# Optimization experiments

Measured on AMD Instinct MI355X. Metric: run time of the kernel, lower is better.

## Reference

```python
import jax, jax.numpy as jnp
import numpy as np

D_MODEL = 1024
NHEAD = 16
HEAD_DIM = D_MODEL // NHEAD
D_FF = 4096
LN_EPS = 1e-5


def _layernorm(x, gamma, beta):
    mu = jnp.mean(x, axis=-1, keepdims=True)
    var = jnp.mean(jnp.square(x - mu), axis=-1, keepdims=True)
    return (x - mu) * jax.lax.rsqrt(var + LN_EPS) * gamma + beta


def setup_inputs() -> dict:
    key = jax.random.key(0)
    ks = jax.random.split(key, 16)
    s = 1.0 / np.sqrt(D_MODEL)
    sf = 1.0 / np.sqrt(D_FF)
    inp = {
        "src": jax.random.normal(ks[0], (2, 2048, D_MODEL), dtype=jnp.float32),
        # projection weights stored [in, out]
        "Wq": jax.random.uniform(ks[1], (D_MODEL, D_MODEL), minval=-s, maxval=s),
        "bq": jax.random.uniform(ks[2], (D_MODEL,), minval=-s, maxval=s),
        "Wk": jax.random.uniform(ks[3], (D_MODEL, D_MODEL), minval=-s, maxval=s),
        "bk": jax.random.uniform(ks[4], (D_MODEL,), minval=-s, maxval=s),
        "Wv": jax.random.uniform(ks[5], (D_MODEL, D_MODEL), minval=-s, maxval=s),
        "bv": jax.random.uniform(ks[6], (D_MODEL,), minval=-s, maxval=s),
        "Wo": jax.random.uniform(ks[7], (D_MODEL, D_MODEL), minval=-s, maxval=s),
        "bo": jax.random.uniform(ks[8], (D_MODEL,), minval=-s, maxval=s),
        "W1": jax.random.uniform(ks[9], (D_MODEL, D_FF), minval=-s, maxval=s),
        "b1": jax.random.uniform(ks[10], (D_FF,), minval=-s, maxval=s),
        "W2": jax.random.uniform(ks[11], (D_FF, D_MODEL), minval=-sf, maxval=sf),
        "b2": jax.random.uniform(ks[12], (D_MODEL,), minval=-sf, maxval=sf),
        "gamma1": jnp.ones((D_MODEL,), jnp.float32),
        "beta1": jnp.zeros((D_MODEL,), jnp.float32),
        "gamma2": jnp.ones((D_MODEL,), jnp.float32),
        "beta2": jnp.zeros((D_MODEL,), jnp.float32),
    }
    return inp


def reference(src, Wq, bq, Wk, bk, Wv, bv, Wo, bo, W1, b1, W2, b2,
              gamma1, beta1, gamma2, beta2):
    B, L, D = src.shape
    H, Hd = NHEAD, HEAD_DIM
    # QKV projections -> [B, H, L, Hd]
    def split_heads(x):
        return x.reshape(B, L, H, Hd).transpose(0, 2, 1, 3)
    Q = split_heads(src @ Wq + bq)
    K = split_heads(src @ Wk + bk)
    V = split_heads(src @ Wv + bv)
    # attention (dropout is eval-mode identity)
    scores = jnp.einsum("bhqd,bhkd->bhqk", Q, K) / np.sqrt(Hd)
    probs = jax.nn.softmax(scores, axis=-1)
    attn = jnp.einsum("bhqk,bhkd->bhqd", probs, V)
    attn = attn.transpose(0, 2, 1, 3).reshape(B, L, D)
    attn = attn @ Wo + bo
    x = _layernorm(src + attn, gamma1, beta1)
    ff = jax.nn.gelu(x @ W1 + b1, approximate=False) @ W2 + b2
    return _layernorm(x + ff, gamma2, beta2)
```

## Files before the change

kernel.cpp:

```cpp
#include <hip/hip_runtime.h>
#include <cstdint>
#include <cstddef>

using short8 = short __attribute__((ext_vector_type(8)));
using f32x4  = float __attribute__((ext_vector_type(4)));

__device__ __forceinline__ unsigned short f2bf(float f) {
  unsigned int u = __float_as_uint(f);
  u += 0x7fffu + ((u >> 16) & 1u);
  return (unsigned short)(u >> 16);
}
__device__ __forceinline__ float bf2f(unsigned short s) {
  return __uint_as_float(((unsigned int)s) << 16);
}
__device__ __forceinline__ unsigned int pack_bf16_rhu(float lo, float hi) {
  unsigned int a = __float_as_uint(lo) + 0x8000u;
  unsigned int b = __float_as_uint(hi) + 0x8000u;
  return __builtin_amdgcn_perm(b, a, 0x07060302u);
}
__device__ __forceinline__ void async16(const void* g, void* l) {
  __builtin_amdgcn_global_load_lds(
      (const __attribute__((address_space(1))) unsigned int*)g,
      (__attribute__((address_space(3))) unsigned int*)l, 16, 0, 0);
}

#define D_MODEL 1024
#define NHEAD   16
#define HEADD   64
#define SEQL    2048
#define NTOK    4096
#define QSCALE  0.18033688011112042f

__global__ __launch_bounds__(256) void cvt_f32_bf16(const float* __restrict__ in,
                                                    unsigned short* __restrict__ out,
                                                    int n4) {
  int i = blockIdx.x * 256 + threadIdx.x;
  if (i >= n4) return;
  float4 v = ((const float4*)in)[i];
  union { unsigned long long u; unsigned int ui[2]; } pk;
  pk.ui[0] = pack_bf16_rhu(v.x, v.y);
  pk.ui[1] = pack_bf16_rhu(v.z, v.w);
  ((unsigned long long*)out)[i] = pk.u;
}

struct TransTab {
  const float* src[6];
  unsigned short* dst[6];
  int R[6], C[6], start[6], shift[6];
};

__global__ __launch_bounds__(256) void transpose_all(TransTab tt) {
  int id = blockIdx.x, m = 0;
#pragma unroll
  for (int i = 1; i < 6; ++i) if (id >= tt.start[i]) m = i;
  const int local = id - tt.start[m];
  const int R = tt.R[m], C = tt.C[m];
  const int bc = (local & ((1 << tt.shift[m]) - 1)) * 32;
  const int br = (local >> tt.shift[m]) * 32;
  const float* in = tt.src[m];
  unsigned short* out = tt.dst[m];
  __shared__ float tile[32][33];
  const int tx = threadIdx.x & 31, ty = threadIdx.x >> 5;
#pragma unroll
  for (int i = 0; i < 32; i += 8)
    tile[ty + i][tx] = in[(size_t)(br + ty + i) * C + bc + tx];
  __syncthreads();
#pragma unroll
  for (int i = 0; i < 32; i += 8)
    out[(size_t)(bc + ty + i) * R + br + tx] = f2bf(tile[tx][ty + i]);
}

template <int MODE>
__global__ __launch_bounds__(256, 4)
void gemm_bt(const unsigned short* __restrict__ A, const unsigned short* __restrict__ B,
             int M, int N, int K, int Kstride,
             const float* __restrict__ bias0, const float* __restrict__ bias1,
             const float* __restrict__ bias2,
             float* __restrict__ outF, unsigned short* __restrict__ outB,
             unsigned short* __restrict__ outQ, unsigned short* __restrict__ outK,
             unsigned short* __restrict__ outVT) {
  __shared__ __align__(16) short sA[128 * 64];
  __shared__ __align__(16) short sB[128 * 64];
  const int tid = threadIdx.x, wave = tid >> 6, lane = tid & 63;
  const int quad = lane >> 4, l16 = lane & 15;
  const int bm = blockIdx.y * 128, bn = blockIdx.x * 128;
  const int koff = blockIdx.z * K;
  const int wr = (wave >> 1) * 64, wc = (wave & 1) * 64;
  const f32x4 zero4 = {0.f, 0.f, 0.f, 0.f};
  f32x4 acc[4][4];
#pragma unroll
  for (int i = 0; i < 4; ++i)
#pragma unroll
    for (int j = 0; j < 4; ++j) acc[i][j] = zero4;

  for (int kt = 0; kt < K; kt += 64) {
    __syncthreads();
#pragma unroll
    for (int j = 0; j < 4; ++j) {
      int c = (wave * 4 + j) * 64 + lane;
      int row = c >> 3, cp = c & 7;
      int gk = koff + kt + ((cp ^ (row & 7)) * 8);
      async16(A + (size_t)(bm + row) * Kstride + gk, &sA[(wave * 4 + j) * 512]);
      async16(B + (size_t)(bn + row) * Kstride + gk, &sB[(wave * 4 + j) * 512]);
    }
    __syncthreads();
#pragma unroll
    for (int kk = 0; kk < 2; ++kk) {
      short8 af[4], bfr[4];
#pragma unroll
      for (int i = 0; i < 4; ++i) {
        int ra = wr + i * 16 + l16;
        af[i] = *(const short8*)&sA[ra * 64 + (((kk * 4 + quad) ^ (ra & 7)) * 8)];
        int rb = wc + i * 16 + l16;
        bfr[i] = *(const short8*)&sB[rb * 64 + (((kk * 4 + quad) ^ (rb & 7)) * 8)];
      }
#pragma unroll
      for (int mi = 0; mi < 4; ++mi)
#pragma unroll
        for (int ni = 0; ni < 4; ++ni)
          acc[mi][ni] = __builtin_amdgcn_mfma_f32_16x16x32_bf16(af[mi], bfr[ni], acc[mi][ni], 0, 0, 0);
    }
  }

#pragma unroll
  for (int mi = 0; mi < 4; ++mi)
#pragma unroll
    for (int ni = 0; ni < 4; ++ni) {
      const int col = bn + wc + ni * 16 + l16;
      const int row0 = bm + wr + mi * 16 + quad * 4;
      if constexpr (MODE == 0) {
        const int b_ = row0 >> 11, l_ = row0 & 2047;
        if (col < 1024) {
          const int hh = col >> 6, dd = col & 63;
          const size_t o = (((size_t)(b_ * NHEAD + hh)) * SEQL + l_) * HEADD + dd;
#pragma unroll
          for (int r = 0; r < 4; ++r)
            outQ[o + (size_t)r * HEADD] = f2bf((acc[mi][ni][r] + bias0[col]) * QSCALE);
        } else if (col < 2048) {
          const int n2 = col - 1024, hh = n2 >> 6, dd = n2 & 63;
          const size_t o = (((size_t)(b_ * NHEAD + hh)) * SEQL + l_) * HEADD + dd;
#pragma unroll
          for (int r = 0; r < 4; ++r)
            outK[o + (size_t)r * HEADD] = f2bf(acc[mi][ni][r] + bias1[n2]);
        } else {
          const int n2 = col - 2048, hh = n2 >> 6, dd = n2 & 63;
          union { unsigned long long u; unsigned short us[4]; } pk;
#pragma unroll
          for (int r = 0; r < 4; ++r) pk.us[r] = f2bf(acc[mi][ni][r] + bias2[n2]);
          *(unsigned long long*)&outVT[(((size_t)(b_ * NHEAD + hh)) * HEADD + dd) * SEQL + l_] = pk.u;
        }
      } else if constexpr (MODE == 1) {
        float* o = outF + (size_t)blockIdx.z * M * N + (size_t)row0 * N + col;
#pragma unroll
        for (int r = 0; r < 4; ++r) o[(size_t)r * N] = acc[mi][ni][r];
      } else {
#pragma unroll
        for (int r = 0; r < 4; ++r) {
          float x = acc[mi][ni][r] + bias0[col];
          float x2 = x * x;
          float z = x * fmaf(0.102944f, x2, 2.302208f);
          float t = __builtin_amdgcn_exp2f(z);
          float gl = x - x * __builtin_amdgcn_rcpf(t + 1.0f);
          outB[(size_t)(row0 + r) * N + col] = f2bf(gl);
        }
      }
    }
}

__global__ __launch_bounds__(256)
void flash_attn(const unsigned short* __restrict__ Qb, const unsigned short* __restrict__ Kb,
                const unsigned short* __restrict__ VTb, unsigned short* __restrict__ attnA) {
  __shared__ __align__(16) short sV[64 * 128];
  __shared__ __align__(16) short sP[128 * 72];
  const int tid = threadIdx.x, wave = tid >> 6, lane = tid & 63;
  const int quad = lane >> 4, l16 = lane & 15;
  const int bh = blockIdx.y;
  const int q0 = blockIdx.x * 128;
  const size_t baseQK = (size_t)bh * SEQL * HEADD;
  const size_t baseV  = (size_t)bh * HEADD * SEQL;

  short8 qf[2][2];
#pragma unroll
  for (int mi = 0; mi < 2; ++mi)
#pragma unroll
    for (int kk = 0; kk < 2; ++kk) {
      int q = q0 + wave * 32 + mi * 16 + l16;
      qf[mi][kk] = *(const short8*)(Qb + baseQK + (size_t)q * HEADD + kk * 32 + quad * 8);
    }

  const f32x4 zero4 = {0.f, 0.f, 0.f, 0.f};
  f32x4 o_acc[2][4];
  float lsum[2] = {0.f, 0.f};
#pragma unroll
  for (int mi = 0; mi < 2; ++mi)
#pragma unroll
    for (int ni = 0; ni < 4; ++ni) o_acc[mi][ni] = zero4;

  for (int t0 = 0; t0 < SEQL; t0 += 128) {
    __syncthreads();
#pragma unroll
    for (int j = 0; j < 4; ++j) {
      int c = (wave * 4 + j) * 64 + lane;
      int d = c >> 4, cp = c & 15;
      int gl = (cp ^ (d & 15)) * 8;
      async16(VTb + baseV + (size_t)d * SEQL + t0 + gl, &sV[(wave * 4 + j) * 512]);
    }
    __syncthreads();

#pragma unroll
    for (int h = 0; h < 2; ++h) {
      f32x4 st[4][2];
#pragma unroll
      for (int kt = 0; kt < 4; ++kt)
#pragma unroll
        for (int mi = 0; mi < 2; ++mi) st[kt][mi] = zero4;
#pragma unroll
      for (int kt = 0; kt < 4; ++kt) {
        const unsigned short* kp =
            Kb + baseQK + (size_t)(t0 + h * 64 + kt * 16 + l16) * HEADD + quad * 8;
        short8 a0 = *(const short8*)(kp);
        short8 a1 = *(const short8*)(kp + 32);
#pragma unroll
        for (int mi = 0; mi < 2; ++mi) {
          st[kt][mi] = __builtin_amdgcn_mfma_f32_16x16x32_bf16(a0, qf[mi][0], st[kt][mi], 0, 0, 0);
          st[kt][mi] = __builtin_amdgcn_mfma_f32_16x16x32_bf16(a1, qf[mi][1], st[kt][mi], 0, 0, 0);
        }
      }
#pragma unroll
      for (int kt = 0; kt < 4; ++kt)
#pragma unroll
        for (int mi = 0; mi < 2; ++mi) {
          float e0 = __builtin_amdgcn_exp2f(st[kt][mi][0]);
          float e1 = __builtin_amdgcn_exp2f(st[kt][mi][1]);
          float e2 = __builtin_amdgcn_exp2f(st[kt][mi][2]);
          float e3 = __builtin_amdgcn_exp2f(st[kt][mi][3]);
          lsum[mi] += (e0 + e1) + (e2 + e3);
          int q = wave * 32 + mi * 16 + l16;
          union { unsigned long long u; unsigned int ui[2]; } pk;
          pk.ui[0] = pack_bf16_rhu(e0, e1);
          pk.ui[1] = pack_bf16_rhu(e2, e3);
          *(unsigned long long*)&sP[q * 72 + kt * 16 + quad * 4] = pk.u;
        }
#pragma unroll
      for (int c = 0; c < 2; ++c) {
        short8 pf[2];
#pragma unroll
        for (int mi = 0; mi < 2; ++mi) {
          int q = wave * 32 + mi * 16 + l16;
          pf[mi] = *(const short8*)&sP[q * 72 + c * 32 + quad * 8];
        }
#pragma unroll
        for (int ni = 0; ni < 4; ++ni) {
          int vrow = ni * 16 + l16;
          short8 vf = *(const short8*)&sV[vrow * 128 + (((h * 8 + c * 4 + quad) ^ (vrow & 15)) * 8)];
#pragma unroll
          for (int mi = 0; mi < 2; ++mi)
            o_acc[mi][ni] = __builtin_amdgcn_mfma_f32_16x16x32_bf16(pf[mi], vf, o_acc[mi][ni], 0, 0, 0);
        }
      }
    }
  }

#pragma unroll
  for (int mi = 0; mi < 2; ++mi) {
    lsum[mi] += __shfl_xor(lsum[mi], 16, 64);
    lsum[mi] += __shfl_xor(lsum[mi], 32, 64);
  }
  const int b_ = bh >> 4, hh = bh & 15;
#pragma unroll
  for (int mi = 0; mi < 2; ++mi)
#pragma unroll
    for (int r = 0; r < 4; ++r) {
      float inv = 1.0f / __shfl(lsum[mi], quad * 4 + r, 64);
      int qrow = q0 + wave * 32 + mi * 16 + quad * 4 + r;
      size_t orow = ((size_t)(b_ * SEQL + qrow)) * D_MODEL + hh * HEADD;
#pragma unroll
      for (int ni = 0; ni < 4; ++ni)
        attnA[orow + ni * 16 + l16] = f2bf(o_acc[mi][ni][r] * inv);
    }
}

__device__ __forceinline__ void ln_core(float x0, float x1, float x2, float x3,
                                        const float* gamma, const float* beta,
                                        int tid, float& y0, float& y1, float& y2, float& y3) {
  float s = x0 + x1 + x2 + x3;
  float q = x0 * x0 + x1 * x1 + x2 * x2 + x3 * x3;
#pragma unroll
  for (int m = 1; m < 64; m <<= 1) {
    s += __shfl_xor(s, m, 64);
    q += __shfl_xor(q, m, 64);
  }
  __shared__ float red[8];
  const int wv = tid >> 6, ln = tid & 63;
  if (ln == 0) { red[wv] = s; red[4 + wv] = q; }
  __syncthreads();
  float S = red[0] + red[1] + red[2] + red[3];
  float Q2 = red[4] + red[5] + red[6] + red[7];
  float mu = S * (1.0f / 1024.0f);
  float var = Q2 * (1.0f / 1024.0f) - mu * mu;
  float rstd = rsqrtf(var + 1e-5f);
  float4 g = ((const float4*)gamma)[tid];
  float4 b = ((const float4*)beta)[tid];
  y0 = (x0 - mu) * rstd * g.x + b.x;
  y1 = (x1 - mu) * rstd * g.y + b.y;
  y2 = (x2 - mu) * rstd * g.z + b.z;
  y3 = (x3 - mu) * rstd * g.w + b.w;
}

__global__ __launch_bounds__(256)
void ln_combine1(const float* __restrict__ p, int nsplit, const float* __restrict__ src,
                 const float* __restrict__ bias, const float* __restrict__ gamma,
                 const float* __restrict__ beta, unsigned short* __restrict__ outB) {
  const int t = blockIdx.x, tid = threadIdx.x;
  const size_t MN = (size_t)NTOK * 1024, base = (size_t)t * 1024;
  float4 a = ((const float4*)(p + base))[tid];
  for (int s = 1; s < nsplit; ++s) {
    float4 b4 = ((const float4*)(p + s * MN + base))[tid];
    a.x += b4.x; a.y += b4.y; a.z += b4.z; a.w += b4.w;
  }
  float4 s4 = ((const float4*)(src + base))[tid];
  float4 bi = ((const float4*)bias)[tid];
  float y0, y1, y2, y3;
  ln_core(a.x + s4.x + bi.x, a.y + s4.y + bi.y,
          a.z + s4.z + bi.z, a.w + s4.w + bi.w,
          gamma, beta, tid, y0, y1, y2, y3);
  union { unsigned long long u; unsigned int ui[2]; } pk;
  pk.ui[0] = (unsigned)f2bf(y0) | ((unsigned)f2bf(y1) << 16);
  pk.ui[1] = (unsigned)f2bf(y2) | ((unsigned)f2bf(y3) << 16);
  ((unsigned long long*)(outB + base))[tid] = pk.u;
}

__global__ __launch_bounds__(256)
void ln_combine2(const float* __restrict__ p, int nsplit, const unsigned short* __restrict__ resB,
                 const float* __restrict__ bias, const float* __restrict__ gamma,
                 const float* __restrict__ beta, float* __restrict__ outF) {
  const int t = blockIdx.x, tid = threadIdx.x;
  const size_t MN = (size_t)NTOK * 1024, base = (size_t)t * 1024;
  float4 a = ((const float4*)(p + base))[tid];
  for (int s = 1; s < nsplit; ++s) {
    float4 b4 = ((const float4*)(p + s * MN + base))[tid];
    a.x += b4.x; a.y += b4.y; a.z += b4.z; a.w += b4.w;
  }
  union { unsigned long long u; unsigned short us[4]; } r;
  r.u = ((const unsigned long long*)(resB + base))[tid];
  float4 bi = ((const float4*)bias)[tid];
  float y0, y1, y2, y3;
  ln_core(a.x + bf2f(r.us[0]) + bi.x, a.y + bf2f(r.us[1]) + bi.y,
          a.z + bf2f(r.us[2]) + bi.z, a.w + bf2f(r.us[3]) + bi.w,
          gamma, beta, tid, y0, y1, y2, y3);
  float4 o = {y0, y1, y2, y3};
  ((float4*)(outF + base))[tid] = o;
}

extern "C" void kernel_launch(void* const* d_in, const int* in_sizes, int n_in,
                              void* d_out, int out_size, void* d_ws, size_t ws_size,
                              hipStream_t stream) {
  const float* src    = (const float*)d_in[0];
  const float* Wq     = (const float*)d_in[1];
  const float* bq     = (const float*)d_in[2];
  const float* Wk     = (const float*)d_in[3];
  const float* bk     = (const float*)d_in[4];
  const float* Wv     = (const float*)d_in[5];
  const float* bv     = (const float*)d_in[6];
  const float* Wo     = (const float*)d_in[7];
  const float* bo     = (const float*)d_in[8];
  const float* W1     = (const float*)d_in[9];
  const float* b1     = (const float*)d_in[10];
  const float* W2     = (const float*)d_in[11];
  const float* b2     = (const float*)d_in[12];
  const float* gamma1 = (const float*)d_in[13];
  const float* beta1  = (const float*)d_in[14];
  const float* gamma2 = (const float*)d_in[15];
  const float* beta2  = (const float*)d_in[16];
  float* out = (float*)d_out;
  (void)in_sizes; (void)n_in; (void)out_size;

  char* p = (char*)d_ws;
  size_t used = 0;
  auto carve = [&](size_t n) {
    char* r = p; size_t a = (n + 255) & ~(size_t)255; p += a; used += a; return r;
  };
  unsigned short* srcB  = (unsigned short*)carve((size_t)NTOK * 1024 * 2);
  unsigned short* WqkvT = (unsigned short*)carve((size_t)3072 * 1024 * 2);
  unsigned short* WoT   = (unsigned short*)carve((size_t)1024 * 1024 * 2);
  unsigned short* W1T   = (unsigned short*)carve((size_t)4096 * 1024 * 2);
  unsigned short* W2T   = (unsigned short*)carve((size_t)1024 * 4096 * 2);
  unsigned short* Qb    = (unsigned short*)carve((size_t)NTOK * 1024 * 2);
  unsigned short* Kb    = (unsigned short*)carve((size_t)NTOK * 1024 * 2);
  unsigned short* VTb   = (unsigned short*)carve((size_t)NTOK * 1024 * 2);
  carve((size_t)NTOK * 1024 * 2);
  unsigned short* xln   = (unsigned short*)carve((size_t)NTOK * 1024 * 2);
  unsigned short* hmid  = (unsigned short*)carve((size_t)NTOK * 4096 * 2);
  unsigned short* attnA = srcB;
  float* partial2 = (float*)Qb;
  const size_t need4 = (size_t)NTOK * 1024 * 4 * 4;
  float* partial4 = (ws_size >= used + need4) ? (float*)carve(need4) : nullptr;
  const int nsplit = partial4 ? 4 : 2;
  float* partial = partial4 ? partial4 : partial2;

  cvt_f32_bf16<<<4096, 256, 0, stream>>>(src, srcB, NTOK * 1024 / 4);
  TransTab tt;
  tt.src[0] = Wq; tt.src[1] = Wk; tt.src[2] = Wv; tt.src[3] = Wo; tt.src[4] = W1; tt.src[5] = W2;
  tt.dst[0] = WqkvT; tt.dst[1] = WqkvT + 1024 * 1024; tt.dst[2] = WqkvT + 2 * 1024 * 1024;
  tt.dst[3] = WoT; tt.dst[4] = W1T; tt.dst[5] = W2T;
  for (int i = 0; i < 4; ++i) { tt.R[i] = 1024; tt.C[i] = 1024; tt.shift[i] = 5; }
  tt.R[4] = 1024; tt.C[4] = 4096; tt.shift[4] = 7;
  tt.R[5] = 4096; tt.C[5] = 1024; tt.shift[5] = 5;
  tt.start[0] = 0; tt.start[1] = 1024; tt.start[2] = 2048; tt.start[3] = 3072;
  tt.start[4] = 4096; tt.start[5] = 8192;
  transpose_all<<<12288, 256, 0, stream>>>(tt);

  gemm_bt<0><<<dim3(24, 32, 1), 256, 0, stream>>>(srcB, WqkvT, NTOK, 3072, 1024, 1024,
                                                  bq, bk, bv, nullptr, nullptr, Qb, Kb, VTb);
  flash_attn<<<dim3(16, 32), 256, 0, stream>>>(Qb, Kb, VTb, attnA);
  gemm_bt<1><<<dim3(8, 32, nsplit), 256, 0, stream>>>(attnA, WoT, NTOK, 1024, 1024 / nsplit, 1024,
                                                      nullptr, nullptr, nullptr, partial,
                                                      nullptr, nullptr, nullptr, nullptr);
  ln_combine1<<<NTOK, 256, 0, stream>>>(partial, nsplit, src, bo, gamma1, beta1, xln);
  gemm_bt<2><<<dim3(32, 32, 1), 256, 0, stream>>>(xln, W1T, NTOK, 4096, 1024, 1024,
                                                  b1, nullptr, nullptr, nullptr, hmid,
                                                  nullptr, nullptr, nullptr);
  gemm_bt<1><<<dim3(8, 32, nsplit), 256, 0, stream>>>(hmid, W2T, NTOK, 1024, 4096 / nsplit, 4096,
                                                      nullptr, nullptr, nullptr, partial,
                                                      nullptr, nullptr, nullptr, nullptr);
  ln_combine2<<<NTOK, 256, 0, stream>>>(partial, nsplit, xln, b2, gamma2, beta2, out);
}
```

Measured before the change: 391.9 us.

## Split attention keys across wave pairs, stage K/Q in LDS, fuse prep kernels

Flash attention now runs 512-thread blocks where pairs of waves split each 128-key tile and combine partial outputs and row sums through LDS at the end. Q and K tiles are loaded asynchronously into swizzled LDS instead of read per-wave from global memory. The bf16 conversion of src is merged into the weight transpose kernel to drop a launch, and the output-projection/FFN2 split-K is fixed at 2, removing the optional 4-way partial buffer. The key split adds a final reduction and more LDS use per block.

Result: faster. 338.1 us (-13.7%).

```diff
diff --git a/kernel.cpp b/kernel.cpp
--- a/kernel.cpp
+++ b/kernel.cpp
@@ -31,26 +31,28 @@
 #define NTOK    4096
 #define QSCALE  0.18033688011112042f
 
-__global__ __launch_bounds__(256) void cvt_f32_bf16(const float* __restrict__ in,
-                                                    unsigned short* __restrict__ out,
-                                                    int n4) {
-  int i = blockIdx.x * 256 + threadIdx.x;
-  if (i >= n4) return;
-  float4 v = ((const float4*)in)[i];
-  union { unsigned long long u; unsigned int ui[2]; } pk;
-  pk.ui[0] = pack_bf16_rhu(v.x, v.y);
-  pk.ui[1] = pack_bf16_rhu(v.z, v.w);
-  ((unsigned long long*)out)[i] = pk.u;
-}
-
 struct TransTab {
   const float* src[6];
   unsigned short* dst[6];
   int R[6], C[6], start[6], shift[6];
+  const float* cvt_in;
+  unsigned short* cvt_out;
 };
 
-__global__ __launch_bounds__(256) void transpose_all(TransTab tt) {
-  int id = blockIdx.x, m = 0;
+__global__ __launch_bounds__(256) void prep_all(TransTab tt) {
+  __shared__ float tile[32][33];
+  int id = blockIdx.x;
+  if (id < 4096) {
+    int i = id * 256 + threadIdx.x;
+    float4 v = ((const float4*)tt.cvt_in)[i];
+    union { unsigned long long u; unsigned int ui[2]; } pk;
+    pk.ui[0] = pack_bf16_rhu(v.x, v.y);
+    pk.ui[1] = pack_bf16_rhu(v.z, v.w);
+    ((unsigned long long*)tt.cvt_out)[i] = pk.u;
+    return;
+  }
+  id -= 4096;
+  int m = 0;
 #pragma unroll
   for (int i = 1; i < 6; ++i) if (id >= tt.start[i]) m = i;
   const int local = id - tt.start[m];
@@ -59,7 +61,6 @@
   const int br = (local >> tt.shift[m]) * 32;
   const float* in = tt.src[m];
   unsigned short* out = tt.dst[m];
-  __shared__ float tile[32][33];
   const int tx = threadIdx.x & 31, ty = threadIdx.x >> 5;
 #pragma unroll
   for (int i = 0; i < 32; i += 8)
@@ -167,25 +168,38 @@
     }
 }
 
-__global__ __launch_bounds__(256)
+__global__ __launch_bounds__(512, 4)
 void flash_attn(const unsigned short* __restrict__ Qb, const unsigned short* __restrict__ Kb,
                 const unsigned short* __restrict__ VTb, unsigned short* __restrict__ attnA) {
+  __shared__ __align__(16) short sK[128 * 64];
   __shared__ __align__(16) short sV[64 * 128];
-  __shared__ __align__(16) short sP[128 * 72];
+  __shared__ __align__(16) short sP[8 * 32 * 72];
+  __shared__ float lred[4][32];
   const int tid = threadIdx.x, wave = tid >> 6, lane = tid & 63;
   const int quad = lane >> 4, l16 = lane & 15;
+  const int wq = wave >> 1;
+  const int wk = wave & 1;
   const int bh = blockIdx.y;
   const int q0 = blockIdx.x * 128;
   const size_t baseQK = (size_t)bh * SEQL * HEADD;
   const size_t baseV  = (size_t)bh * HEADD * SEQL;
-
+  const int pbase = wave * (32 * 72);
+
+#pragma unroll
+  for (int j = 0; j < 2; ++j) {
+    int c = (wave * 2 + j) * 64 + lane;
+    int row = c >> 3, cp = c & 7;
+    int gk = (cp ^ (row & 7)) * 8;
+    async16(Qb + baseQK + (size_t)(q0 + row) * HEADD + gk, &sK[(wave * 2 + j) * 512]);
+  }
+  __syncthreads();
   short8 qf[2][2];
 #pragma unroll
   for (int mi = 0; mi < 2; ++mi)
 #pragma unroll
     for (int kk = 0; kk < 2; ++kk) {
-      int q = q0 + wave * 32 + mi * 16 + l16;
-      qf[mi][kk] = *(const short8*)(Qb + baseQK + (size_t)q * HEADD + kk * 32 + quad * 8);
+      int m = wq * 32 + mi * 16 + l16;
+      qf[mi][kk] = *(const short8*)&sK[m * 64 + (((kk * 4 + quad) ^ (m & 7)) * 8)];
     }
 
   const f32x4 zero4 = {0.f, 0.f, 0.f, 0.f};
@@ -199,64 +213,61 @@
   for (int t0 = 0; t0 < SEQL; t0 += 128) {
     __syncthreads();
 #pragma unroll
-    for (int j = 0; j < 4; ++j) {
-      int c = (wave * 4 + j) * 64 + lane;
-      int d = c >> 4, cp = c & 15;
-      int gl = (cp ^ (d & 15)) * 8;
-      async16(VTb + baseV + (size_t)d * SEQL + t0 + gl, &sV[(wave * 4 + j) * 512]);
+    for (int j = 0; j < 2; ++j) {
+      int c = (wave * 2 + j) * 64 + lane;
+      { int row = c >> 3, cp = c & 7;
+        int gk = (cp ^ (row & 7)) * 8;
+        async16(Kb + baseQK + (size_t)(t0 + row) * HEADD + gk, &sK[(wave * 2 + j) * 512]); }
+      { int d = c >> 4, cp = c & 15;
+        int gl = (cp ^ (d & 15)) * 8;
+        async16(VTb + baseV + (size_t)d * SEQL + t0 + gl, &sV[(wave * 2 + j) * 512]); }
     }
     __syncthreads();
 
-#pragma unroll
-    for (int h = 0; h < 2; ++h) {
-      f32x4 st[4][2];
-#pragma unroll
-      for (int kt = 0; kt < 4; ++kt)
-#pragma unroll
-        for (int mi = 0; mi < 2; ++mi) st[kt][mi] = zero4;
-#pragma unroll
-      for (int kt = 0; kt < 4; ++kt) {
-        const unsigned short* kp =
-            Kb + baseQK + (size_t)(t0 + h * 64 + kt * 16 + l16) * HEADD + quad * 8;
-        short8 a0 = *(const short8*)(kp);
-        short8 a1 = *(const short8*)(kp + 32);
-#pragma unroll
-        for (int mi = 0; mi < 2; ++mi) {
-          st[kt][mi] = __builtin_amdgcn_mfma_f32_16x16x32_bf16(a0, qf[mi][0], st[kt][mi], 0, 0, 0);
-          st[kt][mi] = __builtin_amdgcn_mfma_f32_16x16x32_bf16(a1, qf[mi][1], st[kt][mi], 0, 0, 0);
-        }
-      }
-#pragma unroll
-      for (int kt = 0; kt < 4; ++kt)
-#pragma unroll
-        for (int mi = 0; mi < 2; ++mi) {
-          float e0 = __builtin_amdgcn_exp2f(st[kt][mi][0]);
-          float e1 = __builtin_amdgcn_exp2f(st[kt][mi][1]);
-          float e2 = __builtin_amdgcn_exp2f(st[kt][mi][2]);
-          float e3 = __builtin_amdgcn_exp2f(st[kt][mi][3]);
-          lsum[mi] += (e0 + e1) + (e2 + e3);
-          int q = wave * 32 + mi * 16 + l16;
-          union { unsigned long long u; unsigned int ui[2]; } pk;
-          pk.ui[0] = pack_bf16_rhu(e0, e1);
-          pk.ui[1] = pack_bf16_rhu(e2, e3);
-          *(unsigned long long*)&sP[q * 72 + kt * 16 + quad * 4] = pk.u;
-        }
-#pragma unroll
-      for (int c = 0; c < 2; ++c) {
-        short8 pf[2];
-#pragma unroll
-        for (int mi = 0; mi < 2; ++mi) {
-          int q = wave * 32 + mi * 16 + l16;
-          pf[mi] = *(const short8*)&sP[q * 72 + c * 32 + quad * 8];
-        }
-#pragma unroll
-        for (int ni = 0; ni < 4; ++ni) {
-          int vrow = ni * 16 + l16;
-          short8 vf = *(const short8*)&sV[vrow * 128 + (((h * 8 + c * 4 + quad) ^ (vrow & 15)) * 8)];
-#pragma unroll
-          for (int mi = 0; mi < 2; ++mi)
-            o_acc[mi][ni] = __builtin_amdgcn_mfma_f32_16x16x32_bf16(pf[mi], vf, o_acc[mi][ni], 0, 0, 0);
-        }
+    f32x4 st[4][2];
+#pragma unroll
+    for (int kt = 0; kt < 4; ++kt)
+#pragma unroll
+      for (int mi = 0; mi < 2; ++mi) st[kt][mi] = zero4;
+#pragma unroll
+    for (int kt = 0; kt < 4; ++kt) {
+      int krow = wk * 64 + kt * 16 + l16;
+      short8 a0 = *(const short8*)&sK[krow * 64 + ((quad ^ (krow & 7)) * 8)];
+      short8 a1 = *(const short8*)&sK[krow * 64 + (((4 + quad) ^ (krow & 7)) * 8)];
+#pragma unroll
+      for (int mi = 0; mi < 2; ++mi) {
+        st[kt][mi] = __builtin_amdgcn_mfma_f32_16x16x32_bf16(a0, qf[mi][0], st[kt][mi], 0, 0, 0);
+        st[kt][mi] = __builtin_amdgcn_mfma_f32_16x16x32_bf16(a1, qf[mi][1], st[kt][mi], 0, 0, 0);
+      }
+    }
+#pragma unroll
+    for (int kt = 0; kt < 4; ++kt)
+#pragma unroll
+      for (int mi = 0; mi < 2; ++mi) {
+        float e0 = __builtin_amdgcn_exp2f(st[kt][mi][0]);
+        float e1 = __builtin_amdgcn_exp2f(st[kt][mi][1]);
+        float e2 = __builtin_amdgcn_exp2f(st[kt][mi][2]);
+        float e3 = __builtin_amdgcn_exp2f(st[kt][mi][3]);
+        lsum[mi] += (e0 + e1) + (e2 + e3);
+        union { unsigned long long u; unsigned int ui[2]; } pk;
+        pk.ui[0] = pack_bf16_rhu(e0, e1);
+        pk.ui[1] = pack_bf16_rhu(e2, e3);
+        *(unsigned long long*)&sP[pbase + (mi * 16 + l16) * 72 + kt * 16 + quad * 4] = pk.u;
+      }
+#pragma unroll
+    for (int c = 0; c < 2; ++c) {
+      short8 vf[4];
+#pragma unroll
+      for (int ni = 0; ni < 4; ++ni) {
+        int vrow = ni * 16 + l16;
+        vf[ni] = *(const short8*)&sV[vrow * 128 + (((wk * 8 + c * 4 + quad) ^ (vrow & 15)) * 8)];
+      }
+#pragma unroll
+      for (int mi = 0; mi < 2; ++mi) {
+        short8 pf = *(const short8*)&sP[pbase + (mi * 16 + l16) * 72 + c * 32 + quad * 8];
+#pragma unroll
+        for (int ni = 0; ni < 4; ++ni)
+          o_acc[mi][ni] = __builtin_amdgcn_mfma_f32_16x16x32_bf16(pf, vf[ni], o_acc[mi][ni], 0, 0, 0);
       }
     }
   }
@@ -266,18 +277,43 @@
     lsum[mi] += __shfl_xor(lsum[mi], 16, 64);
     lsum[mi] += __shfl_xor(lsum[mi], 32, 64);
   }
-  const int b_ = bh >> 4, hh = bh & 15;
-#pragma unroll
-  for (int mi = 0; mi < 2; ++mi)
-#pragma unroll
-    for (int r = 0; r < 4; ++r) {
-      float inv = 1.0f / __shfl(lsum[mi], quad * 4 + r, 64);
-      int qrow = q0 + wave * 32 + mi * 16 + quad * 4 + r;
-      size_t orow = ((size_t)(b_ * SEQL + qrow)) * D_MODEL + hh * HEADD;
+  __syncthreads();
+  float* op = (float*)sP;
+  if (wk == 1) {
+    float* dst = op + wq * (64 * 36);
+#pragma unroll
+    for (int mi = 0; mi < 2; ++mi)
 #pragma unroll
       for (int ni = 0; ni < 4; ++ni)
-        attnA[orow + ni * 16 + l16] = f2bf(o_acc[mi][ni][r] * inv);
-    }
+        *(f32x4*)&dst[(ni * 16 + l16) * 36 + mi * 16 + quad * 4] = o_acc[mi][ni];
+    if (quad == 0) {
+      lred[wq][l16] = lsum[0];
+      lred[wq][16 + l16] = lsum[1];
+    }
+  }
+  __syncthreads();
+  if (wk == 0) {
+    const float* srcp = op + wq * (64 * 36);
+    const int b_ = bh >> 4, hh = bh & 15;
+#pragma unroll
+    for (int mi = 0; mi < 2; ++mi) {
+      float ltot = lsum[mi] + lred[wq][mi * 16 + l16];
+#pragma unroll
+      for (int ni = 0; ni < 4; ++ni) {
+        f32x4 other = *(const f32x4*)&srcp[(ni * 16 + l16) * 36 + mi * 16 + quad * 4];
+        o_acc[mi][ni] += other;
+      }
+#pragma unroll
+      for (int r = 0; r < 4; ++r) {
+        float inv = 1.0f / __shfl(ltot, quad * 4 + r, 64);
+        int qrow = q0 + wq * 32 + mi * 16 + quad * 4 + r;
+        size_t orow = ((size_t)(b_ * SEQL + qrow)) * D_MODEL + hh * HEADD;
+#pragma unroll
+        for (int ni = 0; ni < 4; ++ni)
+          attnA[orow + ni * 16 + l16] = f2bf(o_acc[mi][ni][r] * inv);
+      }
+    }
+  }
 }
 
 __device__ __forceinline__ void ln_core(float x0, float x1, float x2, float x3,
@@ -308,16 +344,14 @@
 }
 
 __global__ __launch_bounds__(256)
-void ln_combine1(const float* __restrict__ p, int nsplit, const float* __restrict__ src,
+void ln_combine1(const float* __restrict__ p, const float* __restrict__ src,
                  const float* __restrict__ bias, const float* __restrict__ gamma,
                  const float* __restrict__ beta, unsigned short* __restrict__ outB) {
   const int t = blockIdx.x, tid = threadIdx.x;
   const size_t MN = (size_t)NTOK * 1024, base = (size_t)t * 1024;
   float4 a = ((const float4*)(p + base))[tid];
-  for (int s = 1; s < nsplit; ++s) {
-    float4 b4 = ((const float4*)(p + s * MN + base))[tid];
-    a.x += b4.x; a.y += b4.y; a.z += b4.z; a.w += b4.w;
-  }
+  float4 b4 = ((const float4*)(p + MN + base))[tid];
+  a.x += b4.x; a.y += b4.y; a.z += b4.z; a.w += b4.w;
   float4 s4 = ((const float4*)(src + base))[tid];
   float4 bi = ((const float4*)bias)[tid];
   float y0, y1, y2, y3;
@@ -331,16 +365,14 @@
 }
 
 __global__ __launch_bounds__(256)
-void ln_combine2(const float* __restrict__ p, int nsplit, const unsigned short* __restrict__ resB,
+void ln_combine2(const float* __restrict__ p, const unsigned short* __restrict__ resB,
                  const float* __restrict__ bias, const float* __restrict__ gamma,
                  const float* __restrict__ beta, float* __restrict__ outF) {
   const int t = blockIdx.x, tid = threadIdx.x;
   const size_t MN = (size_t)NTOK * 1024, base = (size_t)t * 1024;
   float4 a = ((const float4*)(p + base))[tid];
-  for (int s = 1; s < nsplit; ++s) {
-    float4 b4 = ((const float4*)(p + s * MN + base))[tid];
-    a.x += b4.x; a.y += b4.y; a.z += b4.z; a.w += b4.w;
-  }
+  float4 b4 = ((const float4*)(p + MN + base))[tid];
+  a.x += b4.x; a.y += b4.y; a.z += b4.z; a.w += b4.w;
   union { unsigned long long u; unsigned short us[4]; } r;
   r.u = ((const unsigned long long*)(resB + base))[tid];
   float4 bi = ((const float4*)bias)[tid];
@@ -373,13 +405,10 @@
   const float* gamma2 = (const float*)d_in[15];
   const float* beta2  = (const float*)d_in[16];
   float* out = (float*)d_out;
-  (void)in_sizes; (void)n_in; (void)out_size;
+  (void)in_sizes; (void)n_in; (void)out_size; (void)ws_size;
 
   char* p = (char*)d_ws;
-  size_t used = 0;
-  auto carve = [&](size_t n) {
-    char* r = p; size_t a = (n + 255) & ~(size_t)255; p += a; used += a; return r;
-  };
+  auto carve = [&](size_t n) { char* r = p; p += (n + 255) & ~(size_t)255; return r; };
   unsigned short* srcB  = (unsigned short*)carve((size_t)NTOK * 1024 * 2);
   unsigned short* WqkvT = (unsigned short*)carve((size_t)3072 * 1024 * 2);
   unsigned short* WoT   = (unsigned short*)carve((size_t)1024 * 1024 * 2);
@@ -392,13 +421,8 @@
   unsigned short* xln   = (unsigned short*)carve((size_t)NTOK * 1024 * 2);
   unsigned short* hmid  = (unsigned short*)carve((size_t)NTOK * 4096 * 2);
   unsigned short* attnA = srcB;
-  float* partial2 = (float*)Qb;
-  const size_t need4 = (size_t)NTOK * 1024 * 4 * 4;
-  float* partial4 = (ws_size >= used + need4) ? (float*)carve(need4) : nullptr;
-  const int nsplit = partial4 ? 4 : 2;
-  float* partial = partial4 ? partial4 : partial2;
-
-  cvt_f32_bf16<<<4096, 256, 0, stream>>>(src, srcB, NTOK * 1024 / 4);
+  float* partial = (float*)Qb;
+
   TransTab tt;
   tt.src[0] = Wq; tt.src[1] = Wk; tt.src[2] = Wv; tt.src[3] = Wo; tt.src[4] = W1; tt.src[5] = W2;
   tt.dst[0] = WqkvT; tt.dst[1] = WqkvT + 1024 * 1024; tt.dst[2] = WqkvT + 2 * 1024 * 1024;
@@ -408,20 +432,21 @@
   tt.R[5] = 4096; tt.C[5] = 1024; tt.shift[5] = 5;
   tt.start[0] = 0; tt.start[1] = 1024; tt.start[2] = 2048; tt.start[3] = 3072;
   tt.start[4] = 4096; tt.start[5] = 8192;
-  transpose_all<<<12288, 256, 0, stream>>>(tt);
+  tt.cvt_in = src; tt.cvt_out = srcB;
+  prep_all<<<16384, 256, 0, stream>>>(tt);
 
   gemm_bt<0><<<dim3(24, 32, 1), 256, 0, stream>>>(srcB, WqkvT, NTOK, 3072, 1024, 1024,
                                                   bq, bk, bv, nullptr, nullptr, Qb, Kb, VTb);
-  flash_attn<<<dim3(16, 32), 256, 0, stream>>>(Qb, Kb, VTb, attnA);
-  gemm_bt<1><<<dim3(8, 32, nsplit), 256, 0, stream>>>(attnA, WoT, NTOK, 1024, 1024 / nsplit, 1024,
-                                                      nullptr, nullptr, nullptr, partial,
-                                                      nullptr, nullptr, nullptr, nullptr);
-  ln_combine1<<<NTOK, 256, 0, stream>>>(partial, nsplit, src, bo, gamma1, beta1, xln);
+  flash_attn<<<dim3(16, 32), 512, 0, stream>>>(Qb, Kb, VTb, attnA);
+  gemm_bt<1><<<dim3(8, 32, 2), 256, 0, stream>>>(attnA, WoT, NTOK, 1024, 512, 1024,
+                                                 nullptr, nullptr, nullptr, partial,
+                                                 nullptr, nullptr, nullptr, nullptr);
+  ln_combine1<<<NTOK, 256, 0, stream>>>(partial, src, bo, gamma1, beta1, xln);
   gemm_bt<2><<<dim3(32, 32, 1), 256, 0, stream>>>(xln, W1T, NTOK, 4096, 1024, 1024,
                                                   b1, nullptr, nullptr, nullptr, hmid,
                                                   nullptr, nullptr, nullptr);
-  gemm_bt<1><<<dim3(8, 32, nsplit), 256, 0, stream>>>(hmid, W2T, NTOK, 1024, 4096 / nsplit, 4096,
-                                                      nullptr, nullptr, nullptr, partial,
-                                                      nullptr, nullptr, nullptr, nullptr);
-  ln_combine2<<<NTOK, 256, 0, stream>>>(partial, nsplit, xln, b2, gamma2, beta2, out);
-}
+  gemm_bt<1><<<dim3(8, 32, 2), 256, 0, stream>>>(hmid, W2T, NTOK, 1024, 2048, 4096,
+                                                 nullptr, nullptr, nullptr, partial,
+                                                 nullptr, nullptr, nullptr, nullptr);
+  ln_combine2<<<NTOK, 256, 0, stream>>>(partial, xln, b2, gamma2, beta2, out);
+}
```
